# Kernel optimization log

Measured on AMD Instinct MI355X. Metric: run time of the kernel, lower is better.

Reference implementation:

```python
import jax, jax.numpy as jnp
import numpy as np

VOXEL_RES = 4
CLASSES = 40


def setup_inputs() -> dict:
    key = jax.random.key(0)
    kx, kw, kb = jax.random.split(key, 3)
    B, N = 64, 100000
    x = jax.random.normal(kx, (B, N, 3), dtype=jnp.float32)
    F = VOXEL_RES ** 3
    bound = 1.0 / np.sqrt(F)  # torch Linear default init range
    W = jax.random.uniform(kw, (CLASSES, F), minval=-bound, maxval=bound, dtype=jnp.float32)
    b = jax.random.uniform(kb, (CLASSES,), minval=-bound, maxval=bound, dtype=jnp.float32)
    return {"x": x, "W": W, "b": b}


def reference(x, W, b):
    # x: (B, N, 3). Faithful to torch.histogramdd(bins=R): the histogram range
    # per dimension is [min, max] of the data; the last bin is right-inclusive.
    B, N, _ = x.shape
    R = VOXEL_RES
    mn = jnp.min(x, axis=1, keepdims=True)  # (B, 1, 3)
    mx = jnp.max(x, axis=1, keepdims=True)  # (B, 1, 3)
    # bin index = floor((v - min) / (max - min) * R), clipped so v == max -> R-1
    idx = jnp.floor((x - mn) / (mx - mn) * R).astype(jnp.int32)
    idx = jnp.clip(idx, 0, R - 1)  # (B, N, 3)
    flat = idx[..., 0] * R * R + idx[..., 1] * R + idx[..., 2]  # (B, N)
    flat = flat + (jnp.arange(B, dtype=jnp.int32) * (R ** 3))[:, None]
    counts = jax.ops.segment_sum(
        jnp.ones((B * N,), dtype=x.dtype), flat.reshape(-1), num_segments=B * R ** 3
    ).reshape(B, R ** 3)
    counts = counts / N  # fraction of points per voxel
    class_outputs = counts @ W.T + b  # (B, classes)
    return class_outputs
```

## Files before the change

kernel.cpp:

```cpp
#include <hip/hip_runtime.h>

#define VR 4
#define NVOX 64
#define NCLS 40
#define NB 64
#define NPTS 100000
#define BPB 25
#define GPB 1000
#define ATH 250
#define G_PER_B (NPTS / 4)
#define F4_PER_B (NPTS * 3 / 4)
#define FLT_BIG 3.402823466e38f

__global__ __launch_bounds__(256) void minmax_k(const float4* __restrict__ x,
                                                float* __restrict__ pmin,
                                                float* __restrict__ pmax) {
    const int b = blockIdx.x / BPB;
    const int sub = blockIdx.x % BPB;
    const float4* xb = x + (size_t)b * F4_PER_B;
    const int tid = threadIdx.x;
    const int lane = tid & 63;
    const int wv = tid >> 6;
    const int t = tid < ATH ? tid : ATH - 1;

    float4 d[12];
    #pragma unroll
    for (int k = 0; k < 4; ++k) {
        int g = sub * GPB + k * ATH + t;
        d[3 * k + 0] = xb[3 * g + 0];
        d[3 * k + 1] = xb[3 * g + 1];
        d[3 * k + 2] = xb[3 * g + 2];
    }

    float mn0 = FLT_BIG, mn1 = FLT_BIG, mn2 = FLT_BIG;
    float mx0 = -FLT_BIG, mx1 = -FLT_BIG, mx2 = -FLT_BIG;
    if (tid < ATH) {
        #pragma unroll
        for (int k = 0; k < 4; ++k) {
            float4 a = d[3 * k], c = d[3 * k + 1], e = d[3 * k + 2];
            mn0 = fminf(mn0, fminf(fminf(a.x, a.w), fminf(c.z, e.y)));
            mx0 = fmaxf(mx0, fmaxf(fmaxf(a.x, a.w), fmaxf(c.z, e.y)));
            mn1 = fminf(mn1, fminf(fminf(a.y, c.x), fminf(c.w, e.z)));
            mx1 = fmaxf(mx1, fmaxf(fmaxf(a.y, c.x), fmaxf(c.w, e.z)));
            mn2 = fminf(mn2, fminf(fminf(a.z, c.y), fminf(e.x, e.w)));
            mx2 = fmaxf(mx2, fmaxf(fmaxf(a.z, c.y), fmaxf(e.x, e.w)));
        }
    }

    #pragma unroll
    for (int off = 32; off > 0; off >>= 1) {
        mn0 = fminf(mn0, __shfl_down(mn0, off, 64));
        mn1 = fminf(mn1, __shfl_down(mn1, off, 64));
        mn2 = fminf(mn2, __shfl_down(mn2, off, 64));
        mx0 = fmaxf(mx0, __shfl_down(mx0, off, 64));
        mx1 = fmaxf(mx1, __shfl_down(mx1, off, 64));
        mx2 = fmaxf(mx2, __shfl_down(mx2, off, 64));
    }

    __shared__ float smn[4][3], smx[4][3];
    if (lane == 0) {
        smn[wv][0] = mn0; smn[wv][1] = mn1; smn[wv][2] = mn2;
        smx[wv][0] = mx0; smx[wv][1] = mx1; smx[wv][2] = mx2;
    }
    __syncthreads();
    if (tid < 3) {
        const int dd = tid;
        float a = smn[0][dd], z = smx[0][dd];
        #pragma unroll
        for (int w = 1; w < 4; w++) {
            a = fminf(a, smn[w][dd]);
            z = fmaxf(z, smx[w][dd]);
        }
        pmin[(b * BPB + sub) * 3 + dd] = a;
        pmax[(b * BPB + sub) * 3 + dd] = z;
    }
}

__device__ __forceinline__ int bin1(float v, float mn, float s4) {
    int i = (int)((v - mn) * s4);
    return i > (VR - 1) ? (VR - 1) : i;
}

__device__ __forceinline__ void tally(int v, unsigned long long vm,
                                      const unsigned long long* ns,
                                      unsigned& cnt) {
    unsigned long long b0 = __ballot(v & 1);
    unsigned long long b1 = __ballot(v & 2);
    unsigned long long b2 = __ballot(v & 4);
    unsigned long long b3 = __ballot(v & 8);
    unsigned long long b4 = __ballot(v & 16);
    unsigned long long b5 = __ballot(v & 32);
    unsigned long long m = vm & (b0 ^ ns[0]) & (b1 ^ ns[1]) & (b2 ^ ns[2])
                              & (b3 ^ ns[3]) & (b4 ^ ns[4]) & (b5 ^ ns[5]);
    cnt += (unsigned)__popcll(m);
}

__global__ __launch_bounds__(256) void hist_k(const float4* __restrict__ x,
                                              const float* __restrict__ pmin,
                                              const float* __restrict__ pmax,
                                              unsigned* __restrict__ phist) {
    const int b = blockIdx.x / BPB;
    const int sub = blockIdx.x % BPB;
    const float4* xb = x + (size_t)b * F4_PER_B;
    const int tid = threadIdx.x;
    const int lane = tid & 63;
    const int wv = tid >> 6;
    const int t = tid < ATH ? tid : ATH - 1;

    float4 d[12];
    #pragma unroll
    for (int k = 0; k < 4; ++k) {
        int g = sub * GPB + k * ATH + t;
        d[3 * k + 0] = xb[3 * g + 0];
        d[3 * k + 1] = xb[3 * g + 1];
        d[3 * k + 2] = xb[3 * g + 2];
    }

    __shared__ float smm[6];
    if (wv < 2) {
        const float* src = (wv == 0) ? pmin : pmax;
        float v0, v1, v2;
        if (lane < BPB) {
            v0 = src[(b * BPB + lane) * 3 + 0];
            v1 = src[(b * BPB + lane) * 3 + 1];
            v2 = src[(b * BPB + lane) * 3 + 2];
        } else {
            v0 = v1 = v2 = (wv == 0) ? FLT_BIG : -FLT_BIG;
        }
        #pragma unroll
        for (int off = 16; off > 0; off >>= 1) {
            float u0 = __shfl_down(v0, off, 64);
            float u1 = __shfl_down(v1, off, 64);
            float u2 = __shfl_down(v2, off, 64);
            if (wv == 0) {
                v0 = fminf(v0, u0); v1 = fminf(v1, u1); v2 = fminf(v2, u2);
            } else {
                v0 = fmaxf(v0, u0); v1 = fmaxf(v1, u1); v2 = fmaxf(v2, u2);
            }
        }
        if (lane == 0) {
            smm[wv * 3 + 0] = v0; smm[wv * 3 + 1] = v1; smm[wv * 3 + 2] = v2;
        }
    }
    __syncthreads();
    const float mn_0 = smm[0], mn_1 = smm[1], mn_2 = smm[2];
    const float s4_0 = (float)VR / (smm[3] - mn_0);
    const float s4_1 = (float)VR / (smm[4] - mn_1);
    const float s4_2 = (float)VR / (smm[5] - mn_2);

    unsigned long long ns[6];
    #pragma unroll
    for (int k = 0; k < 6; k++)
        ns[k] = ((lane >> k) & 1) ? 0ull : ~0ull;
    const unsigned long long vm = __ballot(tid < ATH);

    unsigned c_ = 0;
    #pragma unroll
    for (int k = 0; k < 4; ++k) {
        float4 a = d[3 * k], c = d[3 * k + 1], e = d[3 * k + 2];
        int v0 = bin1(a.x, mn_0, s4_0) * 16 + bin1(a.y, mn_1, s4_1) * 4 + bin1(a.z, mn_2, s4_2);
        int v1 = bin1(a.w, mn_0, s4_0) * 16 + bin1(c.x, mn_1, s4_1) * 4 + bin1(c.y, mn_2, s4_2);
        int v2 = bin1(c.z, mn_0, s4_0) * 16 + bin1(c.w, mn_1, s4_1) * 4 + bin1(e.x, mn_2, s4_2);
        int v3 = bin1(e.y, mn_0, s4_0) * 16 + bin1(e.z, mn_1, s4_1) * 4 + bin1(e.w, mn_2, s4_2);
        tally(v0, vm, ns, c_);
        tally(v1, vm, ns, c_);
        tally(v2, vm, ns, c_);
        tally(v3, vm, ns, c_);
    }

    __shared__ unsigned swh[4][NVOX];
    swh[wv][lane] = c_;
    __syncthreads();
    if (tid < NVOX) {
        phist[(b * BPB + sub) * NVOX + tid] =
            swh[0][tid] + swh[1][tid] + swh[2][tid] + swh[3][tid];
    }
}

__global__ __launch_bounds__(256) void gemv_k(const unsigned* __restrict__ phist,
                                              const float* __restrict__ W,
                                              const float* __restrict__ bias,
                                              float* __restrict__ out) {
    const int b = blockIdx.x;
    __shared__ float fh[NVOX];
    __shared__ float sW[NCLS * NVOX];

    if (threadIdx.x < NVOX) {
        unsigned s = 0;
        for (int p = 0; p < BPB; p++)
            s += phist[(b * BPB + p) * NVOX + threadIdx.x];
        fh[threadIdx.x] = (float)s * (1.0f / (float)NPTS);
    }
    for (int i = threadIdx.x; i < NCLS * NVOX; i += 256)
        sW[i] = W[i];
    __syncthreads();

    if (threadIdx.x < NCLS) {
        const int c = threadIdx.x;
        float acc = 0.f;
        #pragma unroll
        for (int f = 0; f < NVOX; f++)
            acc += fh[f] * sW[c * NVOX + f];
        out[b * NCLS + c] = acc + bias[c];
    }
}

extern "C" void kernel_launch(void* const* d_in, const int* in_sizes, int n_in,
                              void* d_out, int out_size, void* d_ws, size_t ws_size,
                              hipStream_t stream) {
    const float* x = (const float*)d_in[0];
    const float* W = (const float*)d_in[1];
    const float* bias = (const float*)d_in[2];
    float* out = (float*)d_out;

    float* pmin = (float*)d_ws;
    float* pmax = pmin + NB * BPB * 3;
    unsigned* phist = (unsigned*)(pmax + NB * BPB * 3);

    minmax_k<<<NB * BPB, 256, 0, stream>>>((const float4*)x, pmin, pmax);
    hist_k<<<NB * BPB, 256, 0, stream>>>((const float4*)x, pmin, pmax, phist);
    gemv_k<<<NB, 256, 0, stream>>>(phist, W, bias, out);
}
```

Baseline: 131.2 us.

## Fuse minmax, histogram and GEMV into one kernel with one block per batch

Replaces the three launches (min/max partials, histogram partials, GEMV) with a single kernel using one 1024-thread block per batch. Each block loops over its batch's points twice, first for min/max and then for the histogram, and finishes with the linear layer from shared memory. This removes two launches and the global partial buffers. The cost is a grid of only 64 blocks on a GPU with many more CUs, so far fewer waves are in flight to pull the roughly 77 MB input from memory, and each block reads its batch twice in sequence.

```diff
diff --git a/kernel.cpp b/kernel.cpp
--- a/kernel.cpp
+++ b/kernel.cpp
@@ -5,76 +5,12 @@
 #define NCLS 40
 #define NB 64
 #define NPTS 100000
-#define BPB 25
-#define GPB 1000
-#define ATH 250
-#define G_PER_B (NPTS / 4)
-#define F4_PER_B (NPTS * 3 / 4)
+#define G_TOT 25000
+#define F4_PER_B 75000
+#define TPB 1024
+#define FULL_ITERS 6
+#define TAIL 424
 #define FLT_BIG 3.402823466e38f
-
-__global__ __launch_bounds__(256) void minmax_k(const float4* __restrict__ x,
-                                                float* __restrict__ pmin,
-                                                float* __restrict__ pmax) {
-    const int b = blockIdx.x / BPB;
-    const int sub = blockIdx.x % BPB;
-    const float4* xb = x + (size_t)b * F4_PER_B;
-    const int tid = threadIdx.x;
-    const int lane = tid & 63;
-    const int wv = tid >> 6;
-    const int t = tid < ATH ? tid : ATH - 1;
-
-    float4 d[12];
-    #pragma unroll
-    for (int k = 0; k < 4; ++k) {
-        int g = sub * GPB + k * ATH + t;
-        d[3 * k + 0] = xb[3 * g + 0];
-        d[3 * k + 1] = xb[3 * g + 1];
-        d[3 * k + 2] = xb[3 * g + 2];
-    }
-
-    float mn0 = FLT_BIG, mn1 = FLT_BIG, mn2 = FLT_BIG;
-    float mx0 = -FLT_BIG, mx1 = -FLT_BIG, mx2 = -FLT_BIG;
-    if (tid < ATH) {
-        #pragma unroll
-        for (int k = 0; k < 4; ++k) {
-            float4 a = d[3 * k], c = d[3 * k + 1], e = d[3 * k + 2];
-            mn0 = fminf(mn0, fminf(fminf(a.x, a.w), fminf(c.z, e.y)));
-            mx0 = fmaxf(mx0, fmaxf(fmaxf(a.x, a.w), fmaxf(c.z, e.y)));
-            mn1 = fminf(mn1, fminf(fminf(a.y, c.x), fminf(c.w, e.z)));
-            mx1 = fmaxf(mx1, fmaxf(fmaxf(a.y, c.x), fmaxf(c.w, e.z)));
-            mn2 = fminf(mn2, fminf(fminf(a.z, c.y), fminf(e.x, e.w)));
-            mx2 = fmaxf(mx2, fmaxf(fmaxf(a.z, c.y), fmaxf(e.x, e.w)));
-        }
-    }
-
-    #pragma unroll
-    for (int off = 32; off > 0; off >>= 1) {
-        mn0 = fminf(mn0, __shfl_down(mn0, off, 64));
-        mn1 = fminf(mn1, __shfl_down(mn1, off, 64));
-        mn2 = fminf(mn2, __shfl_down(mn2, off, 64));
-        mx0 = fmaxf(mx0, __shfl_down(mx0, off, 64));
-        mx1 = fmaxf(mx1, __shfl_down(mx1, off, 64));
-        mx2 = fmaxf(mx2, __shfl_down(mx2, off, 64));
-    }
-
-    __shared__ float smn[4][3], smx[4][3];
-    if (lane == 0) {
-        smn[wv][0] = mn0; smn[wv][1] = mn1; smn[wv][2] = mn2;
-        smx[wv][0] = mx0; smx[wv][1] = mx1; smx[wv][2] = mx2;
-    }
-    __syncthreads();
-    if (tid < 3) {
-        const int dd = tid;
-        float a = smn[0][dd], z = smx[0][dd];
-        #pragma unroll
-        for (int w = 1; w < 4; w++) {
-            a = fminf(a, smn[w][dd]);
-            z = fmaxf(z, smx[w][dd]);
-        }
-        pmin[(b * BPB + sub) * 3 + dd] = a;
-        pmax[(b * BPB + sub) * 3 + dd] = z;
-    }
-}
 
 __device__ __forceinline__ int bin1(float v, float mn, float s4) {
     int i = (int)((v - mn) * s4);
@@ -95,54 +31,85 @@
     cnt += (unsigned)__popcll(m);
 }
 
-__global__ __launch_bounds__(256) void hist_k(const float4* __restrict__ x,
-                                              const float* __restrict__ pmin,
-                                              const float* __restrict__ pmax,
-                                              unsigned* __restrict__ phist) {
-    const int b = blockIdx.x / BPB;
-    const int sub = blockIdx.x % BPB;
+__global__ __launch_bounds__(TPB) void fused_k(const float4* __restrict__ x,
+                                               const float* __restrict__ W,
+                                               const float* __restrict__ bias,
+                                               float* __restrict__ out) {
+    const int b = blockIdx.x;
     const float4* xb = x + (size_t)b * F4_PER_B;
     const int tid = threadIdx.x;
     const int lane = tid & 63;
     const int wv = tid >> 6;
-    const int t = tid < ATH ? tid : ATH - 1;
 
-    float4 d[12];
-    #pragma unroll
-    for (int k = 0; k < 4; ++k) {
-        int g = sub * GPB + k * ATH + t;
-        d[3 * k + 0] = xb[3 * g + 0];
-        d[3 * k + 1] = xb[3 * g + 1];
-        d[3 * k + 2] = xb[3 * g + 2];
+    __shared__ float sW[NCLS * 65];
+    __shared__ float smn[16][3], smx[16][3];
+    __shared__ float smm[6];
+    __shared__ unsigned swh[16][NVOX];
+    __shared__ float fh[NVOX];
+
+    for (int i = tid; i < NCLS * NVOX; i += TPB)
+        sW[(i >> 6) * 65 + (i & 63)] = W[i];
+
+    float mn0 = FLT_BIG, mn1 = FLT_BIG, mn2 = FLT_BIG;
+    float mx0 = -FLT_BIG, mx1 = -FLT_BIG, mx2 = -FLT_BIG;
+
+    for (int it = 0; it < FULL_ITERS; ++it) {
+        float4 d[12];
+        #pragma unroll
+        for (int k = 0; k < 4; ++k) {
+            int g = it * (4 * TPB) + k * TPB + tid;
+            d[3 * k + 0] = xb[3 * g + 0];
+            d[3 * k + 1] = xb[3 * g + 1];
+            d[3 * k + 2] = xb[3 * g + 2];
+        }
+        #pragma unroll
+        for (int k = 0; k < 4; ++k) {
+            float4 a = d[3 * k], c = d[3 * k + 1], e = d[3 * k + 2];
+            mn0 = fminf(mn0, fminf(fminf(a.x, a.w), fminf(c.z, e.y)));
+            mx0 = fmaxf(mx0, fmaxf(fmaxf(a.x, a.w), fmaxf(c.z, e.y)));
+            mn1 = fminf(mn1, fminf(fminf(a.y, c.x), fminf(c.w, e.z)));
+            mx1 = fmaxf(mx1, fmaxf(fmaxf(a.y, c.x), fmaxf(c.w, e.z)));
+            mn2 = fminf(mn2, fminf(fminf(a.z, c.y), fminf(e.x, e.w)));
+            mx2 = fmaxf(mx2, fmaxf(fmaxf(a.z, c.y), fmaxf(e.x, e.w)));
+        }
+    }
+    if (tid < TAIL) {
+        int g = FULL_ITERS * 4 * TPB + tid;
+        float4 a = xb[3 * g], c = xb[3 * g + 1], e = xb[3 * g + 2];
+        mn0 = fminf(mn0, fminf(fminf(a.x, a.w), fminf(c.z, e.y)));
+        mx0 = fmaxf(mx0, fmaxf(fmaxf(a.x, a.w), fmaxf(c.z, e.y)));
+        mn1 = fminf(mn1, fminf(fminf(a.y, c.x), fminf(c.w, e.z)));
+        mx1 = fmaxf(mx1, fmaxf(fmaxf(a.y, c.x), fmaxf(c.w, e.z)));
+        mn2 = fminf(mn2, fminf(fminf(a.z, c.y), fminf(e.x, e.w)));
+        mx2 = fmaxf(mx2, fmaxf(fmaxf(a.z, c.y), fmaxf(e.x, e.w)));
     }
 
-    __shared__ float smm[6];
-    if (wv < 2) {
-        const float* src = (wv == 0) ? pmin : pmax;
-        float v0, v1, v2;
-        if (lane < BPB) {
-            v0 = src[(b * BPB + lane) * 3 + 0];
-            v1 = src[(b * BPB + lane) * 3 + 1];
-            v2 = src[(b * BPB + lane) * 3 + 2];
-        } else {
-            v0 = v1 = v2 = (wv == 0) ? FLT_BIG : -FLT_BIG;
-        }
-        #pragma unroll
-        for (int off = 16; off > 0; off >>= 1) {
-            float u0 = __shfl_down(v0, off, 64);
-            float u1 = __shfl_down(v1, off, 64);
-            float u2 = __shfl_down(v2, off, 64);
-            if (wv == 0) {
-                v0 = fminf(v0, u0); v1 = fminf(v1, u1); v2 = fminf(v2, u2);
-            } else {
-                v0 = fmaxf(v0, u0); v1 = fmaxf(v1, u1); v2 = fmaxf(v2, u2);
-            }
-        }
-        if (lane == 0) {
-            smm[wv * 3 + 0] = v0; smm[wv * 3 + 1] = v1; smm[wv * 3 + 2] = v2;
-        }
+    #pragma unroll
+    for (int off = 32; off > 0; off >>= 1) {
+        mn0 = fminf(mn0, __shfl_down(mn0, off, 64));
+        mn1 = fminf(mn1, __shfl_down(mn1, off, 64));
+        mn2 = fminf(mn2, __shfl_down(mn2, off, 64));
+        mx0 = fmaxf(mx0, __shfl_down(mx0, off, 64));
+        mx1 = fmaxf(mx1, __shfl_down(mx1, off, 64));
+        mx2 = fmaxf(mx2, __shfl_down(mx2, off, 64));
+    }
+    if (lane == 0) {
+        smn[wv][0] = mn0; smn[wv][1] = mn1; smn[wv][2] = mn2;
+        smx[wv][0] = mx0; smx[wv][1] = mx1; smx[wv][2] = mx2;
     }
     __syncthreads();
+    if (tid < 3) {
+        float a = smn[0][tid], z = smx[0][tid];
+        #pragma unroll
+        for (int w = 1; w < 16; w++) {
+            a = fminf(a, smn[w][tid]);
+            z = fmaxf(z, smx[w][tid]);
+        }
+        smm[tid] = a;
+        smm[3 + tid] = z;
+    }
+    __syncthreads();
+
     const float mn_0 = smm[0], mn_1 = smm[1], mn_2 = smm[2];
     const float s4_0 = (float)VR / (smm[3] - mn_0);
     const float s4_1 = (float)VR / (smm[4] - mn_1);
@@ -152,12 +119,35 @@
     #pragma unroll
     for (int k = 0; k < 6; k++)
         ns[k] = ((lane >> k) & 1) ? 0ull : ~0ull;
-    const unsigned long long vm = __ballot(tid < ATH);
 
     unsigned c_ = 0;
-    #pragma unroll
-    for (int k = 0; k < 4; ++k) {
-        float4 a = d[3 * k], c = d[3 * k + 1], e = d[3 * k + 2];
+    for (int it = 0; it < FULL_ITERS; ++it) {
+        float4 d[12];
+        #pragma unroll
+        for (int k = 0; k < 4; ++k) {
+            int g = it * (4 * TPB) + k * TPB + tid;
+            d[3 * k + 0] = xb[3 * g + 0];
+            d[3 * k + 1] = xb[3 * g + 1];
+            d[3 * k + 2] = xb[3 * g + 2];
+        }
+        #pragma unroll
+        for (int k = 0; k < 4; ++k) {
+            float4 a = d[3 * k], c = d[3 * k + 1], e = d[3 * k + 2];
+            int v0 = bin1(a.x, mn_0, s4_0) * 16 + bin1(a.y, mn_1, s4_1) * 4 + bin1(a.z, mn_2, s4_2);
+            int v1 = bin1(a.w, mn_0, s4_0) * 16 + bin1(c.x, mn_1, s4_1) * 4 + bin1(c.y, mn_2, s4_2);
+            int v2 = bin1(c.z, mn_0, s4_0) * 16 + bin1(c.w, mn_1, s4_1) * 4 + bin1(e.x, mn_2, s4_2);
+            int v3 = bin1(e.y, mn_0, s4_0) * 16 + bin1(e.z, mn_1, s4_1) * 4 + bin1(e.w, mn_2, s4_2);
+            tally(v0, ~0ull, ns, c_);
+            tally(v1, ~0ull, ns, c_);
+            tally(v2, ~0ull, ns, c_);
+            tally(v3, ~0ull, ns, c_);
+        }
+    }
+    if (wv * 64 < TAIL) {
+        bool act = tid < TAIL;
+        int g = act ? (FULL_ITERS * 4 * TPB + tid) : (G_TOT - 1);
+        float4 a = xb[3 * g], c = xb[3 * g + 1], e = xb[3 * g + 2];
+        unsigned long long vm = __ballot(act);
         int v0 = bin1(a.x, mn_0, s4_0) * 16 + bin1(a.y, mn_1, s4_1) * 4 + bin1(a.z, mn_2, s4_2);
         int v1 = bin1(a.w, mn_0, s4_0) * 16 + bin1(c.x, mn_1, s4_1) * 4 + bin1(c.y, mn_2, s4_2);
         int v2 = bin1(c.z, mn_0, s4_0) * 16 + bin1(c.w, mn_1, s4_1) * 4 + bin1(e.x, mn_2, s4_2);
@@ -168,40 +158,22 @@
         tally(v3, vm, ns, c_);
     }
 
-    __shared__ unsigned swh[4][NVOX];
     swh[wv][lane] = c_;
     __syncthreads();
+
     if (tid < NVOX) {
-        phist[(b * BPB + sub) * NVOX + tid] =
-            swh[0][tid] + swh[1][tid] + swh[2][tid] + swh[3][tid];
+        unsigned s = 0;
+        #pragma unroll
+        for (int w = 0; w < 16; w++) s += swh[w][tid];
+        fh[tid] = (float)s * (1.0f / (float)NPTS);
     }
-}
-
-__global__ __launch_bounds__(256) void gemv_k(const unsigned* __restrict__ phist,
-                                              const float* __restrict__ W,
-                                              const float* __restrict__ bias,
-                                              float* __restrict__ out) {
-    const int b = blockIdx.x;
-    __shared__ float fh[NVOX];
-    __shared__ float sW[NCLS * NVOX];
-
-    if (threadIdx.x < NVOX) {
-        unsigned s = 0;
-        for (int p = 0; p < BPB; p++)
-            s += phist[(b * BPB + p) * NVOX + threadIdx.x];
-        fh[threadIdx.x] = (float)s * (1.0f / (float)NPTS);
-    }
-    for (int i = threadIdx.x; i < NCLS * NVOX; i += 256)
-        sW[i] = W[i];
     __syncthreads();
-
-    if (threadIdx.x < NCLS) {
-        const int c = threadIdx.x;
+    if (tid < NCLS) {
         float acc = 0.f;
         #pragma unroll
         for (int f = 0; f < NVOX; f++)
-            acc += fh[f] * sW[c * NVOX + f];
-        out[b * NCLS + c] = acc + bias[c];
+            acc += fh[f] * sW[tid * 65 + f];
+        out[b * NCLS + tid] = acc + bias[tid];
     }
 }
 
@@ -213,11 +185,5 @@
     const float* bias = (const float*)d_in[2];
     float* out = (float*)d_out;
 
-    float* pmin = (float*)d_ws;
-    float* pmax = pmin + NB * BPB * 3;
-    unsigned* phist = (unsigned*)(pmax + NB * BPB * 3);
-
-    minmax_k<<<NB * BPB, 256, 0, stream>>>((const float4*)x, pmin, pmax);
-    hist_k<<<NB * BPB, 256, 0, stream>>>((const float4*)x, pmin, pmax, phist);
-    gemv_k<<<NB, 256, 0, stream>>>(phist, W, bias, out);
+    fused_k<<<NB, TPB, 0, stream>>>((const float4*)x, W, bias, out);
 }
```

New measurement: 173.0 us. 31.9% more time.

## Stage point loads through LDS via global_load_lds with per-wave double buffering

Applied to the files above, without the earlier changes.

Both minmax and histogram kernels now give each wave its own contiguous 750-float4 slice. The slice is streamed into LDS through global_load_lds and double buffered with manual waitcnt, so loads overlap the reduce and tally work. This replaces the earlier strided per-thread register loads, which had an idle tail of threads. The histogram kernel also drops its syncthreads for the min/max broadcast and uses an in-wave xor-shuffle reduction instead. The new path relies on hand-coded waitcnt encodings and uses more LDS per block, which could limit occupancy.

```diff
diff --git a/kernel.cpp b/kernel.cpp
--- a/kernel.cpp
+++ b/kernel.cpp
@@ -6,74 +6,17 @@
 #define NB 64
 #define NPTS 100000
 #define BPB 25
-#define GPB 1000
-#define ATH 250
-#define G_PER_B (NPTS / 4)
-#define F4_PER_B (NPTS * 3 / 4)
+#define WPB 4
+#define GPW 250
+#define F4_PER_B 75000
+#define TAIL_LANES 58
+#define F4_PER_WAVE 750
 #define FLT_BIG 3.402823466e38f
 
-__global__ __launch_bounds__(256) void minmax_k(const float4* __restrict__ x,
-                                                float* __restrict__ pmin,
-                                                float* __restrict__ pmax) {
-    const int b = blockIdx.x / BPB;
-    const int sub = blockIdx.x % BPB;
-    const float4* xb = x + (size_t)b * F4_PER_B;
-    const int tid = threadIdx.x;
-    const int lane = tid & 63;
-    const int wv = tid >> 6;
-    const int t = tid < ATH ? tid : ATH - 1;
-
-    float4 d[12];
-    #pragma unroll
-    for (int k = 0; k < 4; ++k) {
-        int g = sub * GPB + k * ATH + t;
-        d[3 * k + 0] = xb[3 * g + 0];
-        d[3 * k + 1] = xb[3 * g + 1];
-        d[3 * k + 2] = xb[3 * g + 2];
-    }
-
-    float mn0 = FLT_BIG, mn1 = FLT_BIG, mn2 = FLT_BIG;
-    float mx0 = -FLT_BIG, mx1 = -FLT_BIG, mx2 = -FLT_BIG;
-    if (tid < ATH) {
-        #pragma unroll
-        for (int k = 0; k < 4; ++k) {
-            float4 a = d[3 * k], c = d[3 * k + 1], e = d[3 * k + 2];
-            mn0 = fminf(mn0, fminf(fminf(a.x, a.w), fminf(c.z, e.y)));
-            mx0 = fmaxf(mx0, fmaxf(fmaxf(a.x, a.w), fmaxf(c.z, e.y)));
-            mn1 = fminf(mn1, fminf(fminf(a.y, c.x), fminf(c.w, e.z)));
-            mx1 = fmaxf(mx1, fmaxf(fmaxf(a.y, c.x), fmaxf(c.w, e.z)));
-            mn2 = fminf(mn2, fminf(fminf(a.z, c.y), fminf(e.x, e.w)));
-            mx2 = fmaxf(mx2, fmaxf(fmaxf(a.z, c.y), fmaxf(e.x, e.w)));
-        }
-    }
-
-    #pragma unroll
-    for (int off = 32; off > 0; off >>= 1) {
-        mn0 = fminf(mn0, __shfl_down(mn0, off, 64));
-        mn1 = fminf(mn1, __shfl_down(mn1, off, 64));
-        mn2 = fminf(mn2, __shfl_down(mn2, off, 64));
-        mx0 = fmaxf(mx0, __shfl_down(mx0, off, 64));
-        mx1 = fmaxf(mx1, __shfl_down(mx1, off, 64));
-        mx2 = fmaxf(mx2, __shfl_down(mx2, off, 64));
-    }
-
-    __shared__ float smn[4][3], smx[4][3];
-    if (lane == 0) {
-        smn[wv][0] = mn0; smn[wv][1] = mn1; smn[wv][2] = mn2;
-        smx[wv][0] = mx0; smx[wv][1] = mx1; smx[wv][2] = mx2;
-    }
-    __syncthreads();
-    if (tid < 3) {
-        const int dd = tid;
-        float a = smn[0][dd], z = smx[0][dd];
-        #pragma unroll
-        for (int w = 1; w < 4; w++) {
-            a = fminf(a, smn[w][dd]);
-            z = fmaxf(z, smx[w][dd]);
-        }
-        pmin[(b * BPB + sub) * 3 + dd] = a;
-        pmax[(b * BPB + sub) * 3 + dd] = z;
-    }
+__device__ __forceinline__ void gl2lds(const float4* g, float4* l) {
+    __builtin_amdgcn_global_load_lds(
+        (const __attribute__((address_space(1))) void*)g,
+        (__attribute__((address_space(3))) void*)l, 16, 0, 0);
 }
 
 __device__ __forceinline__ int bin1(float v, float mn, float s4) {
@@ -95,6 +38,82 @@
     cnt += (unsigned)__popcll(m);
 }
 
+__global__ __launch_bounds__(256) void minmax_k(const float4* __restrict__ x,
+                                                float* __restrict__ pmin,
+                                                float* __restrict__ pmax) {
+    const int b = blockIdx.x / BPB;
+    const int sub = blockIdx.x % BPB;
+    const float4* xb = x + (size_t)b * F4_PER_B;
+    const int tid = threadIdx.x;
+    const int lane = tid & 63;
+    const int w = tid >> 6;
+    const float4* xw = xb + (size_t)(sub * WPB + w) * F4_PER_WAVE;
+
+    __shared__ float4 stage[WPB][2][192];
+
+    #pragma unroll
+    for (int j = 0; j < 3; ++j)
+        gl2lds(xw + j * 64 + lane, &stage[w][0][j * 64]);
+
+    float mn0 = FLT_BIG, mn1 = FLT_BIG, mn2 = FLT_BIG;
+    float mx0 = -FLT_BIG, mx1 = -FLT_BIG, mx2 = -FLT_BIG;
+
+    #pragma unroll
+    for (int it = 0; it < 4; ++it) {
+        const int cur = it & 1;
+        if (it < 3) {
+            #pragma unroll
+            for (int j = 0; j < 3; ++j) {
+                int o = (it + 1) * 192 + j * 64 + lane;
+                if (o > F4_PER_WAVE - 1) o = F4_PER_WAVE - 1;
+                gl2lds(xw + o, &stage[w][cur ^ 1][j * 64]);
+            }
+            __builtin_amdgcn_s_waitcnt(0x0f73);
+        } else {
+            __builtin_amdgcn_s_waitcnt(0x0f70);
+        }
+        float4 a = stage[w][cur][3 * lane];
+        float4 c = stage[w][cur][3 * lane + 1];
+        float4 e = stage[w][cur][3 * lane + 2];
+        bool act = (it < 3) || (lane < TAIL_LANES);
+        if (act) {
+            mn0 = fminf(mn0, fminf(fminf(a.x, a.w), fminf(c.z, e.y)));
+            mx0 = fmaxf(mx0, fmaxf(fmaxf(a.x, a.w), fmaxf(c.z, e.y)));
+            mn1 = fminf(mn1, fminf(fminf(a.y, c.x), fminf(c.w, e.z)));
+            mx1 = fmaxf(mx1, fmaxf(fmaxf(a.y, c.x), fmaxf(c.w, e.z)));
+            mn2 = fminf(mn2, fminf(fminf(a.z, c.y), fminf(e.x, e.w)));
+            mx2 = fmaxf(mx2, fmaxf(fmaxf(a.z, c.y), fmaxf(e.x, e.w)));
+        }
+    }
+
+    #pragma unroll
+    for (int off = 32; off > 0; off >>= 1) {
+        mn0 = fminf(mn0, __shfl_down(mn0, off, 64));
+        mn1 = fminf(mn1, __shfl_down(mn1, off, 64));
+        mn2 = fminf(mn2, __shfl_down(mn2, off, 64));
+        mx0 = fmaxf(mx0, __shfl_down(mx0, off, 64));
+        mx1 = fmaxf(mx1, __shfl_down(mx1, off, 64));
+        mx2 = fmaxf(mx2, __shfl_down(mx2, off, 64));
+    }
+
+    __shared__ float smn[WPB][3], smx[WPB][3];
+    if (lane == 0) {
+        smn[w][0] = mn0; smn[w][1] = mn1; smn[w][2] = mn2;
+        smx[w][0] = mx0; smx[w][1] = mx1; smx[w][2] = mx2;
+    }
+    __syncthreads();
+    if (tid < 3) {
+        float a = smn[0][tid], z = smx[0][tid];
+        #pragma unroll
+        for (int v = 1; v < WPB; v++) {
+            a = fminf(a, smn[v][tid]);
+            z = fmaxf(z, smx[v][tid]);
+        }
+        pmin[(b * BPB + sub) * 3 + tid] = a;
+        pmax[(b * BPB + sub) * 3 + tid] = z;
+    }
+}
+
 __global__ __launch_bounds__(256) void hist_k(const float4* __restrict__ x,
                                               const float* __restrict__ pmin,
                                               const float* __restrict__ pmax,
@@ -104,72 +123,82 @@
     const float4* xb = x + (size_t)b * F4_PER_B;
     const int tid = threadIdx.x;
     const int lane = tid & 63;
-    const int wv = tid >> 6;
-    const int t = tid < ATH ? tid : ATH - 1;
-
-    float4 d[12];
-    #pragma unroll
-    for (int k = 0; k < 4; ++k) {
-        int g = sub * GPB + k * ATH + t;
-        d[3 * k + 0] = xb[3 * g + 0];
-        d[3 * k + 1] = xb[3 * g + 1];
-        d[3 * k + 2] = xb[3 * g + 2];
-    }
-
-    __shared__ float smm[6];
-    if (wv < 2) {
-        const float* src = (wv == 0) ? pmin : pmax;
-        float v0, v1, v2;
-        if (lane < BPB) {
-            v0 = src[(b * BPB + lane) * 3 + 0];
-            v1 = src[(b * BPB + lane) * 3 + 1];
-            v2 = src[(b * BPB + lane) * 3 + 2];
+    const int w = tid >> 6;
+    const float4* xw = xb + (size_t)(sub * WPB + w) * F4_PER_WAVE;
+
+    __shared__ float4 stage[WPB][2][192];
+
+    #pragma unroll
+    for (int j = 0; j < 3; ++j)
+        gl2lds(xw + j * 64 + lane, &stage[w][0][j * 64]);
+
+    float v0, v1, v2;
+    {
+        bool lo = lane < 32;
+        int s = lo ? lane : lane - 32;
+        if (s < BPB) {
+            const float* src = lo ? pmin : pmax;
+            v0 = src[(b * BPB + s) * 3 + 0];
+            v1 = src[(b * BPB + s) * 3 + 1];
+            v2 = src[(b * BPB + s) * 3 + 2];
         } else {
-            v0 = v1 = v2 = (wv == 0) ? FLT_BIG : -FLT_BIG;
+            v0 = v1 = v2 = lo ? FLT_BIG : -FLT_BIG;
         }
         #pragma unroll
         for (int off = 16; off > 0; off >>= 1) {
-            float u0 = __shfl_down(v0, off, 64);
-            float u1 = __shfl_down(v1, off, 64);
-            float u2 = __shfl_down(v2, off, 64);
-            if (wv == 0) {
-                v0 = fminf(v0, u0); v1 = fminf(v1, u1); v2 = fminf(v2, u2);
-            } else {
-                v0 = fmaxf(v0, u0); v1 = fmaxf(v1, u1); v2 = fmaxf(v2, u2);
-            }
-        }
-        if (lane == 0) {
-            smm[wv * 3 + 0] = v0; smm[wv * 3 + 1] = v1; smm[wv * 3 + 2] = v2;
-        }
-    }
-    __syncthreads();
-    const float mn_0 = smm[0], mn_1 = smm[1], mn_2 = smm[2];
-    const float s4_0 = (float)VR / (smm[3] - mn_0);
-    const float s4_1 = (float)VR / (smm[4] - mn_1);
-    const float s4_2 = (float)VR / (smm[5] - mn_2);
+            float u0 = __shfl_xor(v0, off, 64);
+            float u1 = __shfl_xor(v1, off, 64);
+            float u2 = __shfl_xor(v2, off, 64);
+            v0 = lo ? fminf(v0, u0) : fmaxf(v0, u0);
+            v1 = lo ? fminf(v1, u1) : fmaxf(v1, u1);
+            v2 = lo ? fminf(v2, u2) : fmaxf(v2, u2);
+        }
+    }
+    const float mn_0 = __shfl(v0, 0, 64);
+    const float mn_1 = __shfl(v1, 0, 64);
+    const float mn_2 = __shfl(v2, 0, 64);
+    const float s4_0 = (float)VR / (__shfl(v0, 32, 64) - mn_0);
+    const float s4_1 = (float)VR / (__shfl(v1, 32, 64) - mn_1);
+    const float s4_2 = (float)VR / (__shfl(v2, 32, 64) - mn_2);
 
     unsigned long long ns[6];
     #pragma unroll
     for (int k = 0; k < 6; k++)
         ns[k] = ((lane >> k) & 1) ? 0ull : ~0ull;
-    const unsigned long long vm = __ballot(tid < ATH);
 
     unsigned c_ = 0;
     #pragma unroll
-    for (int k = 0; k < 4; ++k) {
-        float4 a = d[3 * k], c = d[3 * k + 1], e = d[3 * k + 2];
-        int v0 = bin1(a.x, mn_0, s4_0) * 16 + bin1(a.y, mn_1, s4_1) * 4 + bin1(a.z, mn_2, s4_2);
-        int v1 = bin1(a.w, mn_0, s4_0) * 16 + bin1(c.x, mn_1, s4_1) * 4 + bin1(c.y, mn_2, s4_2);
-        int v2 = bin1(c.z, mn_0, s4_0) * 16 + bin1(c.w, mn_1, s4_1) * 4 + bin1(e.x, mn_2, s4_2);
-        int v3 = bin1(e.y, mn_0, s4_0) * 16 + bin1(e.z, mn_1, s4_1) * 4 + bin1(e.w, mn_2, s4_2);
-        tally(v0, vm, ns, c_);
-        tally(v1, vm, ns, c_);
-        tally(v2, vm, ns, c_);
-        tally(v3, vm, ns, c_);
-    }
-
-    __shared__ unsigned swh[4][NVOX];
-    swh[wv][lane] = c_;
+    for (int it = 0; it < 4; ++it) {
+        const int cur = it & 1;
+        if (it < 3) {
+            #pragma unroll
+            for (int j = 0; j < 3; ++j) {
+                int o = (it + 1) * 192 + j * 64 + lane;
+                if (o > F4_PER_WAVE - 1) o = F4_PER_WAVE - 1;
+                gl2lds(xw + o, &stage[w][cur ^ 1][j * 64]);
+            }
+            __builtin_amdgcn_s_waitcnt(0x0f73);
+        } else {
+            __builtin_amdgcn_s_waitcnt(0x0f70);
+        }
+        float4 a = stage[w][cur][3 * lane];
+        float4 c = stage[w][cur][3 * lane + 1];
+        float4 e = stage[w][cur][3 * lane + 2];
+        bool act = (it < 3) || (lane < TAIL_LANES);
+        unsigned long long vm = act ? ~0ull : 0ull;
+        vm = __ballot(act);
+        int p0 = bin1(a.x, mn_0, s4_0) * 16 + bin1(a.y, mn_1, s4_1) * 4 + bin1(a.z, mn_2, s4_2);
+        int p1 = bin1(a.w, mn_0, s4_0) * 16 + bin1(c.x, mn_1, s4_1) * 4 + bin1(c.y, mn_2, s4_2);
+        int p2 = bin1(c.z, mn_0, s4_0) * 16 + bin1(c.w, mn_1, s4_1) * 4 + bin1(e.x, mn_2, s4_2);
+        int p3 = bin1(e.y, mn_0, s4_0) * 16 + bin1(e.z, mn_1, s4_1) * 4 + bin1(e.w, mn_2, s4_2);
+        tally(p0, vm, ns, c_);
+        tally(p1, vm, ns, c_);
+        tally(p2, vm, ns, c_);
+        tally(p3, vm, ns, c_);
+    }
+
+    __shared__ unsigned swh[WPB][NVOX];
+    swh[w][lane] = c_;
     __syncthreads();
     if (tid < NVOX) {
         phist[(b * BPB + sub) * NVOX + tid] =
```

New measurement: 127.0 us. 3.2% less time.
